# Kernel tuning notes

Hardware: AMD Instinct MI355X
Metric: run time of the kernel (lower is better)

## Reference

```python
import jax, jax.numpy as jnp
import numpy as np

N_WIRES = 4


def _apply_rx(state, theta, wire):
    """Apply RX(theta) on `wire`. state: [B] + [2]*n complex; theta: [B] or scalar.
    RX(t) = cos(t/2) I - i sin(t/2) X, and X flips the wire axis."""
    n = state.ndim - 1
    half = theta * 0.5
    c = jnp.cos(half).astype(jnp.complex64)
    s = jnp.sin(half).astype(jnp.complex64)
    c = jnp.reshape(c, jnp.shape(c) + (1,) * n)
    s = jnp.reshape(s, jnp.shape(s) + (1,) * n)
    return c * state - 1j * s * jnp.flip(state, axis=wire + 1)


def _apply_cnot(state, control, target):
    """CNOT: flip target axis on the control=1 slice."""
    s0 = jax.lax.index_in_dim(state, 0, axis=control + 1, keepdims=True)
    s1 = jax.lax.index_in_dim(state, 1, axis=control + 1, keepdims=True)
    s1 = jnp.flip(s1, axis=target + 1)
    return jnp.concatenate([s0, s1], axis=control + 1)


def _encode(data, theta):
    """data: [B, n_wires] float angles -> [B, 2**n_wires] complex state."""
    B = data.shape[0]
    state = jnp.zeros((B,) + (2,) * N_WIRES, dtype=jnp.complex64)
    state = state.at[(slice(None),) + (0,) * N_WIRES].set(1.0)  # |0...0>
    for w in range(N_WIRES):              # data encoding RX per wire
        state = _apply_rx(state, data[:, w], w)
    for w in range(N_WIRES):              # trainable RX per wire
        state = _apply_rx(state, theta[w], w)
    for w in range(N_WIRES - 1):          # CNOT ladder
        state = _apply_cnot(state, w, w + 1)
    return state.reshape(B, 2 ** N_WIRES)


def setup_inputs() -> dict:
    key = jax.random.key(0)
    kx, ky, kt = jax.random.split(key, 3)
    x = jax.random.normal(kx, (8192, 4), dtype=jnp.float32)
    y = jax.random.normal(ky, (8192, 4), dtype=jnp.float32)
    theta = jax.random.normal(kt, (4,), dtype=jnp.float32)
    return {"x": x, "y": y, "theta": theta}


def reference(x, y, theta):
    states_x = _encode(x, theta)  # [Bx, 16] complex64
    states_y = _encode(y, theta)  # [By, 16] complex64
    # Faithful to torch source: plain matmul (no conjugate), then abs.
    return jnp.abs(states_x @ states_y.T)  # [Bx, By] float32
```

## Files before the change

kernel.cpp:

```cpp
#include <hip/hip_runtime.h>
#include <math.h>


#define BM 16
#define BN 256
#define TJ 8

typedef float floatx4 __attribute__((ext_vector_type(4)));

__global__ __launch_bounds__(256) void qk_stream(
    const float* __restrict__ x, const float* __restrict__ y,
    const float* __restrict__ theta, float* __restrict__ out,
    int Nx, int Ny)
{
    const int tid = threadIdx.x;
    const int tx = tid & 63;
    const int ty = tid >> 6;
    const int i0 = blockIdx.y * BM;
    const int j0 = blockIdx.x * (BN * TJ);
    const int r0 = i0 + ty * 4;

    const float th0 = 0.5f * theta[0], th1 = 0.5f * theta[1];
    const float th2 = 0.5f * theta[2], th3 = 0.5f * theta[3];

    float ca[4][4], sa[4][4];
    #pragma unroll
    for (int i = 0; i < 4; ++i) {
        const float4 x4 = ((const float4*)x)[r0 + i];
        __sincosf(0.5f * x4.x + th0, &sa[0][i], &ca[0][i]);
        __sincosf(0.5f * x4.y + th1, &sa[1][i], &ca[1][i]);
        __sincosf(0.5f * x4.z + th2, &sa[2][i], &ca[2][i]);
        __sincosf(0.5f * x4.w + th3, &sa[3][i], &ca[3][i]);
    }

    #pragma unroll 2
    for (int t = 0; t < TJ; ++t) {
        const int j = j0 + t * BN + tx * 4;

        float cb[4][4], sb[4][4];
        #pragma unroll
        for (int jj = 0; jj < 4; ++jj) {
            const float4 y4 = ((const float4*)y)[j + jj];
            __sincosf(0.5f * y4.x + th0, &sb[0][jj], &cb[0][jj]);
            __sincosf(0.5f * y4.y + th1, &sb[1][jj], &cb[1][jj]);
            __sincosf(0.5f * y4.z + th2, &sb[2][jj], &cb[2][jj]);
            __sincosf(0.5f * y4.w + th3, &sb[3][jj], &cb[3][jj]);
        }

        float acc[4][4];
        #pragma unroll
        for (int i = 0; i < 4; ++i) {
            #pragma unroll
            for (int jj = 0; jj < 4; ++jj) {
                const float t0 = fmaf(ca[0][i], cb[0][jj], -(sa[0][i] * sb[0][jj]));
                const float t1 = fmaf(ca[1][i], cb[1][jj], -(sa[1][i] * sb[1][jj]));
                const float t2 = fmaf(ca[2][i], cb[2][jj], -(sa[2][i] * sb[2][jj]));
                const float t3 = fmaf(ca[3][i], cb[3][jj], -(sa[3][i] * sb[3][jj]));
                acc[i][jj] = fabsf((t0 * t1) * (t2 * t3));
            }
        }

        #pragma unroll
        for (int i = 0; i < 4; ++i) {
            floatx4 o;
            o.x = acc[i][0]; o.y = acc[i][1]; o.z = acc[i][2]; o.w = acc[i][3];
            __builtin_nontemporal_store(
                o, (floatx4*)&out[(size_t)(r0 + i) * Ny + j]);
        }
    }
}

__global__ __launch_bounds__(256) void qk_fallback(
    const float* __restrict__ x, const float* __restrict__ y,
    const float* __restrict__ theta, float* __restrict__ out,
    int Bx, int By)
{
    __shared__ float at[8][BM];
    __shared__ float bt[8][BN];

    const int tid = threadIdx.x;
    const int i0 = blockIdx.y * BM;
    const int j0 = blockIdx.x * BN;

    const float th0 = 0.5f * theta[0];
    const float th1 = 0.5f * theta[1];
    const float th2 = 0.5f * theta[2];
    const float th3 = 0.5f * theta[3];

    {
        const float4 y4 = ((const float4*)y)[j0 + tid];
        float s, c;
        __sincosf(0.5f * y4.x + th0, &s, &c); bt[0][tid] = c; bt[4][tid] = s;
        __sincosf(0.5f * y4.y + th1, &s, &c); bt[1][tid] = c; bt[5][tid] = s;
        __sincosf(0.5f * y4.z + th2, &s, &c); bt[2][tid] = c; bt[6][tid] = s;
        __sincosf(0.5f * y4.w + th3, &s, &c); bt[3][tid] = c; bt[7][tid] = s;
    }
    if (tid < BM) {
        const float4 x4 = ((const float4*)x)[i0 + tid];
        float s, c;
        __sincosf(0.5f * x4.x + th0, &s, &c); at[0][tid] = c; at[4][tid] = s;
        __sincosf(0.5f * x4.y + th1, &s, &c); at[1][tid] = c; at[5][tid] = s;
        __sincosf(0.5f * x4.z + th2, &s, &c); at[2][tid] = c; at[6][tid] = s;
        __sincosf(0.5f * x4.w + th3, &s, &c); at[3][tid] = c; at[7][tid] = s;
    }
    __syncthreads();

    const int tx = tid & 63;
    const int ty = tid >> 6;

    float acc[4][4];
    #pragma unroll
    for (int w = 0; w < 4; ++w) {
        const float4 ca = ((const float4*)&at[w][0])[ty];
        const float4 sa = ((const float4*)&at[w + 4][0])[ty];
        const float4 cb = ((const float4*)&bt[w][0])[tx];
        const float4 sb = ((const float4*)&bt[w + 4][0])[tx];

        const float cai[4] = {ca.x, ca.y, ca.z, ca.w};
        const float sai[4] = {sa.x, sa.y, sa.z, sa.w};
        const float cbj[4] = {cb.x, cb.y, cb.z, cb.w};
        const float sbj[4] = {sb.x, sb.y, sb.z, sb.w};

        #pragma unroll
        for (int i = 0; i < 4; ++i) {
            #pragma unroll
            for (int j = 0; j < 4; ++j) {
                const float t = fmaf(cai[i], cbj[j], -(sai[i] * sbj[j]));
                acc[i][j] = (w == 0) ? t : acc[i][j] * t;
            }
        }
    }

    #pragma unroll
    for (int i = 0; i < 4; ++i) {
        const int row = i0 + ty * 4 + i;
        float4 o;
        o.x = fabsf(acc[i][0]);
        o.y = fabsf(acc[i][1]);
        o.z = fabsf(acc[i][2]);
        o.w = fabsf(acc[i][3]);
        ((float4*)&out[(size_t)row * By + j0])[tx] = o;
    }
}

extern "C" void kernel_launch(void* const* d_in, const int* in_sizes, int n_in,
                              void* d_out, int out_size, void* d_ws, size_t ws_size,
                              hipStream_t stream) {
    (void)n_in; (void)out_size; (void)d_ws; (void)ws_size;
    const float* x     = (const float*)d_in[0];
    const float* y     = (const float*)d_in[1];
    const float* theta = (const float*)d_in[2];
    float* out = (float*)d_out;

    const int Bx = in_sizes[0] / 4;
    const int By = in_sizes[1] / 4;

    if ((By % (BN * TJ)) == 0 && (Bx % BM) == 0) {
        dim3 grid(By / (BN * TJ), Bx / BM);
        qk_stream<<<grid, dim3(256), 0, stream>>>(x, y, theta, out, Bx, By);
    } else {
        dim3 grid(By / BN, Bx / BM);
        qk_fallback<<<grid, dim3(256), 0, stream>>>(x, y, theta, out, Bx, By);
    }
}
```

Baseline: 267.0 us.

## Add persistent wave-sweep kernel writing contiguous output chunks

Adds a qk_sweep kernel that launches a fixed set of 8192 waves. Each wave caches the sin/cos terms for its 256 y-columns in registers, then walks down rows with stride NWAVES/cpr, prefetching the next x row while computing the current one. The goal is to give the write stream a contiguous, evenly spread access pattern across the whole output with little per-wave setup. It also drops the nontemporal stores in qk_stream and removes the fallback kernel, which now routes to qk_stream with a possibly wrong grid for shapes that don't divide evenly.

```diff
diff --git a/kernel.cpp b/kernel.cpp
--- a/kernel.cpp
+++ b/kernel.cpp
@@ -5,8 +5,66 @@
 #define BM 16
 #define BN 256
 #define TJ 8
+#define NWAVES 8192
 
 typedef float floatx4 __attribute__((ext_vector_type(4)));
+
+__global__ __launch_bounds__(256) void qk_sweep(
+    const float* __restrict__ x, const float* __restrict__ y,
+    const float* __restrict__ theta, float* __restrict__ out,
+    int Bx, int By, int steps)
+{
+    const int tid  = threadIdx.x;
+    const int lane = tid & 63;
+    const int wid  = (blockIdx.x << 2) + (tid >> 6);
+    const int cpr  = By >> 8;
+    const int jc   = wid % cpr;
+    const int i0   = wid / cpr;
+    const int di   = NWAVES / cpr;
+    const int col0 = jc * 256 + lane * 4;
+
+    const float th0 = 0.5f * theta[0], th1 = 0.5f * theta[1];
+    const float th2 = 0.5f * theta[2], th3 = 0.5f * theta[3];
+
+    float cb[4][4], sb[4][4];
+    #pragma unroll
+    for (int jj = 0; jj < 4; ++jj) {
+        const float4 y4 = ((const float4*)y)[col0 + jj];
+        __sincosf(0.5f * y4.x + th0, &sb[0][jj], &cb[0][jj]);
+        __sincosf(0.5f * y4.y + th1, &sb[1][jj], &cb[1][jj]);
+        __sincosf(0.5f * y4.z + th2, &sb[2][jj], &cb[2][jj]);
+        __sincosf(0.5f * y4.w + th3, &sb[3][jj], &cb[3][jj]);
+    }
+
+    float4 xc = ((const float4*)x)[i0];
+    size_t chunk = (size_t)wid;
+
+    for (int k = 0; k < steps; ++k) {
+        float4 xn;
+        if (k + 1 < steps) xn = ((const float4*)x)[i0 + (k + 1) * di];
+
+        float caw[4], saw[4];
+        __sincosf(0.5f * xc.x + th0, &saw[0], &caw[0]);
+        __sincosf(0.5f * xc.y + th1, &saw[1], &caw[1]);
+        __sincosf(0.5f * xc.z + th2, &saw[2], &caw[2]);
+        __sincosf(0.5f * xc.w + th3, &saw[3], &caw[3]);
+
+        floatx4 o;
+        #pragma unroll
+        for (int jj = 0; jj < 4; ++jj) {
+            const float t0 = fmaf(caw[0], cb[0][jj], -(saw[0] * sb[0][jj]));
+            const float t1 = fmaf(caw[1], cb[1][jj], -(saw[1] * sb[1][jj]));
+            const float t2 = fmaf(caw[2], cb[2][jj], -(saw[2] * sb[2][jj]));
+            const float t3 = fmaf(caw[3], cb[3][jj], -(saw[3] * sb[3][jj]));
+            o[jj] = fabsf((t0 * t1) * (t2 * t3));
+        }
+
+        *(floatx4*)&out[chunk * 256 + (size_t)(lane * 4)] = o;
+
+        chunk += NWAVES;
+        xc = xn;
+    }
+}
 
 __global__ __launch_bounds__(256) void qk_stream(
     const float* __restrict__ x, const float* __restrict__ y,
@@ -62,84 +120,10 @@
 
         #pragma unroll
         for (int i = 0; i < 4; ++i) {
-            floatx4 o;
+            float4 o;
             o.x = acc[i][0]; o.y = acc[i][1]; o.z = acc[i][2]; o.w = acc[i][3];
-            __builtin_nontemporal_store(
-                o, (floatx4*)&out[(size_t)(r0 + i) * Ny + j]);
+            *(float4*)&out[(size_t)(r0 + i) * Ny + j] = o;
         }
-    }
-}
-
-__global__ __launch_bounds__(256) void qk_fallback(
-    const float* __restrict__ x, const float* __restrict__ y,
-    const float* __restrict__ theta, float* __restrict__ out,
-    int Bx, int By)
-{
-    __shared__ float at[8][BM];
-    __shared__ float bt[8][BN];
-
-    const int tid = threadIdx.x;
-    const int i0 = blockIdx.y * BM;
-    const int j0 = blockIdx.x * BN;
-
-    const float th0 = 0.5f * theta[0];
-    const float th1 = 0.5f * theta[1];
-    const float th2 = 0.5f * theta[2];
-    const float th3 = 0.5f * theta[3];
-
-    {
-        const float4 y4 = ((const float4*)y)[j0 + tid];
-        float s, c;
-        __sincosf(0.5f * y4.x + th0, &s, &c); bt[0][tid] = c; bt[4][tid] = s;
-        __sincosf(0.5f * y4.y + th1, &s, &c); bt[1][tid] = c; bt[5][tid] = s;
-        __sincosf(0.5f * y4.z + th2, &s, &c); bt[2][tid] = c; bt[6][tid] = s;
-        __sincosf(0.5f * y4.w + th3, &s, &c); bt[3][tid] = c; bt[7][tid] = s;
-    }
-    if (tid < BM) {
-        const float4 x4 = ((const float4*)x)[i0 + tid];
-        float s, c;
-        __sincosf(0.5f * x4.x + th0, &s, &c); at[0][tid] = c; at[4][tid] = s;
-        __sincosf(0.5f * x4.y + th1, &s, &c); at[1][tid] = c; at[5][tid] = s;
-        __sincosf(0.5f * x4.z + th2, &s, &c); at[2][tid] = c; at[6][tid] = s;
-        __sincosf(0.5f * x4.w + th3, &s, &c); at[3][tid] = c; at[7][tid] = s;
-    }
-    __syncthreads();
-
-    const int tx = tid & 63;
-    const int ty = tid >> 6;
-
-    float acc[4][4];
-    #pragma unroll
-    for (int w = 0; w < 4; ++w) {
-        const float4 ca = ((const float4*)&at[w][0])[ty];
-        const float4 sa = ((const float4*)&at[w + 4][0])[ty];
-        const float4 cb = ((const float4*)&bt[w][0])[tx];
-        const float4 sb = ((const float4*)&bt[w + 4][0])[tx];
-
-        const float cai[4] = {ca.x, ca.y, ca.z, ca.w};
-        const float sai[4] = {sa.x, sa.y, sa.z, sa.w};
-        const float cbj[4] = {cb.x, cb.y, cb.z, cb.w};
-        const float sbj[4] = {sb.x, sb.y, sb.z, sb.w};
-
-        #pragma unroll
-        for (int i = 0; i < 4; ++i) {
-            #pragma unroll
-            for (int j = 0; j < 4; ++j) {
-                const float t = fmaf(cai[i], cbj[j], -(sai[i] * sbj[j]));
-                acc[i][j] = (w == 0) ? t : acc[i][j] * t;
-            }
-        }
-    }
-
-    #pragma unroll
-    for (int i = 0; i < 4; ++i) {
-        const int row = i0 + ty * 4 + i;
-        float4 o;
-        o.x = fabsf(acc[i][0]);
-        o.y = fabsf(acc[i][1]);
-        o.z = fabsf(acc[i][2]);
-        o.w = fabsf(acc[i][3]);
-        ((float4*)&out[(size_t)row * By + j0])[tx] = o;
     }
 }
 
@@ -155,11 +139,21 @@
     const int Bx = in_sizes[0] / 4;
     const int By = in_sizes[1] / 4;
 
+    if ((By % 256) == 0) {
+        const int cpr = By >> 8;
+        const long long chunks = (long long)Bx * cpr;
+        if ((NWAVES % cpr) == 0 && (chunks % NWAVES) == 0 && (By % 1024) == 0) {
+            const int steps = (int)(chunks / NWAVES);
+            qk_sweep<<<dim3(NWAVES / 4), dim3(256), 0, stream>>>(
+                x, y, theta, out, Bx, By, steps);
+            return;
+        }
+    }
     if ((By % (BN * TJ)) == 0 && (Bx % BM) == 0) {
         dim3 grid(By / (BN * TJ), Bx / BM);
         qk_stream<<<grid, dim3(256), 0, stream>>>(x, y, theta, out, Bx, By);
-    } else {
-        dim3 grid(By / BN, Bx / BM);
-        qk_fallback<<<grid, dim3(256), 0, stream>>>(x, y, theta, out, Bx, By);
+        return;
     }
+    dim3 grid(By / BN, Bx / BM);
+    qk_stream<<<grid, dim3(256), 0, stream>>>(x, y, theta, out, Bx, By);
 }
```

Measured after the change: 279.9 us. +4.8%, slower.
